# Kernel tuning notes

Hardware: AMD Instinct MI355X
Metric: run time of the kernel (lower is better)

## Reference

```python
import jax, jax.numpy as jnp
import numpy as np
import math

MARGIN = 0.5
SCALE = 64.0
CURVATURE = 1.0
COS_M = math.cos(MARGIN)
SIN_M = math.sin(MARGIN)
TH = math.cos(math.pi - MARGIN)
MM = math.sin(math.pi - MARGIN) * MARGIN

B, D, C = 2048, 512, 16384


def setup_inputs() -> dict:
    key = jax.random.key(0)
    k1, k2, k3 = jax.random.split(key, 3)
    embeddings = jax.random.normal(k1, (B, D), dtype=jnp.float32) * 0.05  # roughly inside the ball
    labels = jax.random.randint(k2, (B,), 0, C)
    # xavier_uniform for [C, D]
    limit = math.sqrt(6.0 / (C + D))
    weight = jax.random.uniform(k3, (C, D), dtype=jnp.float32, minval=-limit, maxval=limit)
    return {"embeddings": embeddings, "labels": labels, "weight": weight}


def _exp_map_zero(v, c):
    sqrt_c = c ** 0.5
    v_norm = jnp.maximum(jnp.linalg.norm(v, axis=-1, keepdims=True), 1e-7)
    return jnp.tanh(sqrt_c * v_norm) * v / (sqrt_c * v_norm)


def reference(embeddings, labels, weight):
    c = CURVATURE
    # class prototypes mapped onto the Poincare ball, clipped to radius 0.95
    proto = _exp_map_zero(weight, c)                                  # [C, D]
    proto_norm = jnp.linalg.norm(proto, axis=-1, keepdims=True)
    proto = jnp.where(proto_norm > 0.95, proto * 0.95 / proto_norm, proto)

    x = embeddings                                                     # [B, D]
    x_sq = jnp.sum(x * x, axis=-1)                                    # [B]
    y_sq = jnp.sum(proto * proto, axis=-1)                            # [C]
    xy = x @ proto.T                                                  # [B, C]
    diff_sq = jnp.maximum(x_sq[:, None] + y_sq[None, :] - 2.0 * xy, 0.0)

    x_sq_c = jnp.minimum(x_sq, 1.0 - 1e-5)
    y_sq_c = jnp.minimum(y_sq, 1.0 - 1e-5)
    denom = (1.0 - c * x_sq_c)[:, None] * (1.0 - c * y_sq_c)[None, :]
    arg = 1.0 + 2.0 * c * diff_sq / jnp.maximum(denom, 1e-7)
    dists = jnp.arccosh(jnp.maximum(arg, 1.0 + 1e-7)) / (c ** 0.5)    # [B, C]

    sims = jnp.exp(-dists)
    cosine = jnp.clip(2.0 * sims - 1.0, -1.0, 1.0)
    sine = jnp.sqrt(jnp.maximum(1.0 - cosine * cosine, 1e-7))
    phi = cosine * COS_M - sine * SIN_M
    phi = jnp.where(cosine > TH, phi, cosine - MM)

    one_hot = jax.nn.one_hot(labels, cosine.shape[1], dtype=cosine.dtype)
    logits = (one_hot * phi + (1.0 - one_hot) * cosine) * SCALE        # [B, C]

    logp = jax.nn.log_softmax(logits, axis=-1)
    loss = -jnp.mean(jnp.take_along_axis(logp, labels[:, None], axis=1))
    return loss
```

## Files before the change

### kernel.cpp

```cpp
#include <hip/hip_runtime.h>
#include <hip/hip_bf16.h>
#include <math.h>

#define Bn 2048
#define Dn 512
#define Cn 16384

typedef __bf16 v8bf __attribute__((ext_vector_type(8)));
typedef float v4f __attribute__((ext_vector_type(4)));

#define WG_BARRIER() asm volatile("s_waitcnt lgkmcnt(0)\n\ts_barrier" ::: "memory")

__global__ __launch_bounds__(256) void prep_kernel(
    const float* __restrict__ w, const float* __restrict__ x,
    __hip_bfloat16* __restrict__ wbf, __hip_bfloat16* __restrict__ xbf,
    float* __restrict__ fscale, float* __restrict__ ysqA, float* __restrict__ yrA,
    float* __restrict__ xsA, float* __restrict__ xrA)
{
  int gw = (blockIdx.x * 256 + threadIdx.x) >> 6;
  int lane = threadIdx.x & 63;
  bool isW = gw < Cn;
  const float* src = isW ? (w + (size_t)gw * Dn) : (x + (size_t)(gw - Cn) * Dn);
  const float4* s4 = (const float4*)src;
  float4 a = s4[lane * 2], b = s4[lane * 2 + 1];
  float ss = a.x * a.x + a.y * a.y + a.z * a.z + a.w * a.w
           + b.x * b.x + b.y * b.y + b.z * b.z + b.w * b.w;
  #pragma unroll
  for (int d = 1; d < 64; d <<= 1) ss += __shfl_xor(ss, d);

  union { __hip_bfloat16 h[8]; int4 i4; } u;
  u.h[0] = __float2bfloat16(a.x); u.h[1] = __float2bfloat16(a.y);
  u.h[2] = __float2bfloat16(a.z); u.h[3] = __float2bfloat16(a.w);
  u.h[4] = __float2bfloat16(b.x); u.h[5] = __float2bfloat16(b.y);
  u.h[6] = __float2bfloat16(b.z); u.h[7] = __float2bfloat16(b.w);
  __hip_bfloat16* dst = isW ? (wbf + (size_t)gw * Dn) : (xbf + (size_t)(gw - Cn) * Dn);
  ((int4*)dst)[lane] = u.i4;

  if (lane == 0) {
    if (isW) {
      float n = fmaxf(sqrtf(ss), 1e-7f);
      float t = tanhf(n);
      float tc = fminf(t, 0.95f);
      fscale[gw] = tc / n;
      float ys = tc * tc;
      ysqA[gw] = ys;
      yrA[gw] = 1.f / (1.f - fminf(ys, 1.f - 1e-5f));
    } else {
      int r = gw - Cn;
      xsA[r] = ss;
      xrA[r] = 1.f / (1.f - fminf(ss, 1.f - 1e-5f));
    }
  }
}

__global__ __launch_bounds__(256) void gemm_kernel(
    const __hip_bfloat16* __restrict__ xbf, const __hip_bfloat16* __restrict__ wbf,
    const float* __restrict__ fscale, const float* __restrict__ ysqA,
    const float* __restrict__ yrA, const float* __restrict__ xsA,
    const float* __restrict__ xrA, float* __restrict__ partials)
{
  __shared__ int4 ldsv[2048];
  char* lds = (char*)ldsv;

  const int bid = blockIdx.x;
  const int xcd = bid & 7;
  const int loc = bid >> 3;
  const int mt  = loc & 15;
  const int nt  = (xcd << 4) | (loc >> 4);
  const int mBase = mt * 128;
  const int nBase = nt * 128;
  const int tid = threadIdx.x;
  const int lane = tid & 63;
  const int wave = tid >> 6;
  const int quad = lane >> 4;
  const int l16 = lane & 15;
  const int waveM = wave >> 1;
  const int waveN = wave & 1;

  v4f acc[4][4];
  #pragma unroll
  for (int i = 0; i < 4; ++i)
    #pragma unroll
    for (int j = 0; j < 4; ++j)
      acc[i][j] = (v4f){0.f, 0.f, 0.f, 0.f};

  const int r0 = tid >> 2,          c0g = tid & 3;
  const int r1 = (tid + 256) >> 2,  c1g = tid & 3;
  const char* gA0 = (const char*)xbf + (size_t)(mBase + r0) * (Dn * 2) + c0g * 16;
  const char* gA1 = (const char*)xbf + (size_t)(mBase + r1) * (Dn * 2) + c1g * 16;
  const char* gW0 = (const char*)wbf + (size_t)(nBase + r0) * (Dn * 2) + c0g * 16;
  const char* gW1 = (const char*)wbf + (size_t)(nBase + r1) * (Dn * 2) + c1g * 16;
  const int lo0 = r0 * 64 + ((c0g ^ (r0 & 3)) * 16);
  const int lo1 = r1 * 64 + ((c1g ^ (r1 & 3)) * 16);

  int aoffs[4], boffs[4];
  #pragma unroll
  for (int i = 0; i < 4; ++i) {
    int ra = waveM * 64 + i * 16 + l16;
    aoffs[i] = ra * 64 + ((quad ^ (ra & 3)) * 16);
    int rb = waveN * 64 + i * 16 + l16;
    boffs[i] = rb * 64 + ((quad ^ (rb & 3)) * 16);
  }

  int4 tA[2][2], tW[2][2];
  tA[0][0] = *(const int4*)gA0;        tA[0][1] = *(const int4*)gA1;
  tW[0][0] = *(const int4*)gW0;        tW[0][1] = *(const int4*)gW1;
  *(int4*)(lds + lo0) = tA[0][0];      *(int4*)(lds + lo1) = tA[0][1];
  *(int4*)(lds + 8192 + lo0) = tW[0][0]; *(int4*)(lds + 8192 + lo1) = tW[0][1];
  tA[1][0] = *(const int4*)(gA0 + 64);  tA[1][1] = *(const int4*)(gA1 + 64);
  tW[1][0] = *(const int4*)(gW0 + 64);  tW[1][1] = *(const int4*)(gW1 + 64);
  tA[0][0] = *(const int4*)(gA0 + 128); tA[0][1] = *(const int4*)(gA1 + 128);
  tW[0][0] = *(const int4*)(gW0 + 128); tW[0][1] = *(const int4*)(gW1 + 128);

  #pragma unroll
  for (int kt = 0; kt < 16; ++kt) {
    const int cur = kt & 1;
    WG_BARRIER();
    const char* Ab = lds + cur * 16384;
    const char* Wb = Ab + 8192;
    v8bf af[4], bfr[4];
    #pragma unroll
    for (int i = 0; i < 4; ++i) af[i] = *(const v8bf*)(Ab + aoffs[i]);
    #pragma unroll
    for (int j = 0; j < 4; ++j) bfr[j] = *(const v8bf*)(Wb + boffs[j]);
    if (kt < 15) {
      const int par = (kt + 1) & 1;
      char* An = lds + (cur ^ 1) * 16384;
      *(int4*)(An + lo0) = tA[par][0];
      *(int4*)(An + lo1) = tA[par][1];
      *(int4*)(An + 8192 + lo0) = tW[par][0];
      *(int4*)(An + 8192 + lo1) = tW[par][1];
      if (kt + 3 < 16) {
        tA[par][0] = *(const int4*)(gA0 + (kt + 3) * 64);
        tA[par][1] = *(const int4*)(gA1 + (kt + 3) * 64);
        tW[par][0] = *(const int4*)(gW0 + (kt + 3) * 64);
        tW[par][1] = *(const int4*)(gW1 + (kt + 3) * 64);
      }
    }
    #pragma unroll
    for (int i = 0; i < 4; ++i)
      #pragma unroll
      for (int j = 0; j < 4; ++j)
        acc[i][j] = __builtin_amdgcn_mfma_f32_16x16x32_bf16(af[i], bfr[j], acc[i][j], 0, 0, 0);
  }

  float ysqj[4], yrj[4], gj[4];
  #pragma unroll
  for (int j = 0; j < 4; ++j) {
    int col = nBase + waveN * 64 + j * 16 + l16;
    gj[j] = -2.f * fscale[col];
    ysqj[j] = ysqA[col];
    yrj[j] = yrA[col];
  }
  #pragma unroll
  for (int i = 0; i < 4; ++i) {
    #pragma unroll
    for (int r = 0; r < 4; ++r) {
      int row = mBase + waveM * 64 + i * 16 + quad * 4 + r;
      float xs = xsA[row];
      float xr2 = 2.f * xrA[row];
      float partial = 0.f;
      if (xs >= 0.99999f) {
        #pragma unroll
        for (int j = 0; j < 4; ++j) {
          float d = fmaxf(fmaf(gj[j], acc[i][j][r], xs + ysqj[j]), 0.f);
          float z = fmaf(d, xr2 * yrj[j], 1.f);
          float u = 64.f * __builtin_amdgcn_rcpf(z);
          partial += fmaf(u, fmaf(0.5f, u, 1.f), 1.f);
        }
      } else {
        #pragma unroll
        for (int j = 0; j < 4; ++j) {
          float d = fmaxf(fmaf(gj[j], acc[i][j][r], xs + ysqj[j]), 0.f);
          float z = fmaf(d, xr2 * yrj[j], 1.f);
          float sq = sqrtf(fmaf(z, z, -1.f));
          float u = 128.f * __builtin_amdgcn_rcpf(z + sq);
          partial += __expf(u);
        }
      }
      partial += __shfl_xor(partial, 1);
      partial += __shfl_xor(partial, 2);
      partial += __shfl_xor(partial, 4);
      partial += __shfl_xor(partial, 8);
      if (l16 == 0) partials[(size_t)row * 256 + nt * 2 + waveN] = partial;
    }
  }
}

__global__ __launch_bounds__(256) void final_kernel(
    const float* __restrict__ x, const float* __restrict__ w,
    const int* __restrict__ labels, const float* __restrict__ fscale,
    const float* __restrict__ ysqA, const float* __restrict__ yrA,
    const float* __restrict__ xsA, const float* __restrict__ xrA,
    const float* __restrict__ partials, float* __restrict__ out)
{
  int row = blockIdx.x * 4 + (threadIdx.x >> 6);
  int lane = threadIdx.x & 63;
  const float* pr = partials + (size_t)row * 256;
  float sum = pr[lane] + pr[lane + 64] + pr[lane + 128] + pr[lane + 192];

  int lab = labels[row];
  const float4* xv = (const float4*)(x + (size_t)row * Dn);
  const float4* wv = (const float4*)(w + (size_t)lab * Dn);
  float4 a0 = xv[lane * 2], a1 = xv[lane * 2 + 1];
  float4 b0 = wv[lane * 2], b1 = wv[lane * 2 + 1];
  float dot = a0.x * b0.x + a0.y * b0.y + a0.z * b0.z + a0.w * b0.w
            + a1.x * b1.x + a1.y * b1.y + a1.z * b1.z + a1.w * b1.w;
  #pragma unroll
  for (int d = 1; d < 64; d <<= 1) {
    sum += __shfl_xor(sum, d);
    dot += __shfl_xor(dot, d);
  }

  __shared__ float red[4];
  if (lane == 0) {
    float xy = fscale[lab] * dot;
    float diff = fmaxf(xsA[row] + ysqA[lab] - 2.f * xy, 0.f);
    float z = fmaf(2.f * diff, xrA[row] * yrA[lab], 1.f);
    float sq = sqrtf(fmaf(z, z, -1.f));
    float sims = 1.f / (z + sq);
    float u_lab = 128.f * sims;
    float cosv = fmaf(2.f, sims, -1.f);
    float sine = sqrtf(fmaxf(fmaf(-cosv, cosv, 1.f), 1e-7f));
    float phi = (cosv > -0.8775825619f)
                    ? (cosv * 0.8775825619f - sine * 0.4794255386f)
                    : (cosv - 0.2397127693f);
    float e_lab = __expf(u_lab);
    float e_phi = __expf(fminf(64.f * phi + 64.f, 80.f));
    red[threadIdx.x >> 6] = logf(sum - e_lab + e_phi) - 64.f * phi - 64.f;
  }
  __syncthreads();
  if (threadIdx.x == 0)
    atomicAdd(out, (red[0] + red[1] + red[2] + red[3]) * (1.f / (float)Bn));
}

extern "C" void kernel_launch(void* const* d_in, const int* in_sizes, int n_in,
                              void* d_out, int out_size, void* d_ws, size_t ws_size,
                              hipStream_t stream) {
  (void)in_sizes; (void)n_in; (void)out_size; (void)ws_size;
  const float* emb = (const float*)d_in[0];
  const int* labels = (const int*)d_in[1];
  const float* weight = (const float*)d_in[2];
  float* out = (float*)d_out;

  char* p = (char*)d_ws;
  __hip_bfloat16* wbf = (__hip_bfloat16*)p; p += (size_t)Cn * Dn * 2;
  __hip_bfloat16* xbf = (__hip_bfloat16*)p; p += (size_t)Bn * Dn * 2;
  float* fscale = (float*)p; p += (size_t)Cn * 4;
  float* ysqA  = (float*)p; p += (size_t)Cn * 4;
  float* yrA   = (float*)p; p += (size_t)Cn * 4;
  float* xsA   = (float*)p; p += (size_t)Bn * 4;
  float* xrA   = (float*)p; p += (size_t)Bn * 4;
  float* partials = (float*)p; p += (size_t)Bn * 256 * 4;

  hipMemsetAsync(out, 0, sizeof(float), stream);
  prep_kernel<<<(Cn + Bn) / 4, 256, 0, stream>>>(weight, emb, wbf, xbf, fscale, ysqA, yrA, xsA, xrA);
  gemm_kernel<<<(Bn / 128) * (Cn / 128), 256, 0, stream>>>(
      xbf, wbf, fscale, ysqA, yrA, xsA, xrA, partials);
  final_kernel<<<Bn / 4, 256, 0, stream>>>(emb, weight, labels, fscale, ysqA, yrA, xsA, xrA, partials, out);
}
```

Baseline: 148.0 us.

## Stream GEMM tiles into LDS with async global_load_lds double buffering

Replaces the register-staged global-to-LDS copy in the fused distance GEMM with direct global_load_lds transfers into a double-buffered LDS ring, prefetching two k-steps ahead. The XOR swizzle moves from the LDS write address to the global read address, and synchronization becomes vmcnt waits plus barriers. This is meant to free registers and VALU/LDS-write instructions and to overlap loads with MFMA. In exchange it adds an extra barrier per k-step, and the fixed vmcnt(4) count ties correctness to the compiler emitting no other vector memory ops in the loop.

Result: faster. 141.6 us (-4.3%).

```diff
diff --git a/kernel.cpp b/kernel.cpp
--- a/kernel.cpp
+++ b/kernel.cpp
@@ -9,7 +9,16 @@
 typedef __bf16 v8bf __attribute__((ext_vector_type(8)));
 typedef float v4f __attribute__((ext_vector_type(4)));
 
-#define WG_BARRIER() asm volatile("s_waitcnt lgkmcnt(0)\n\ts_barrier" ::: "memory")
+#define WAIT_VM4()      asm volatile("s_waitcnt vmcnt(4)" ::: "memory")
+#define WAIT_VM0()      asm volatile("s_waitcnt vmcnt(0)" ::: "memory")
+#define RAW_BAR()       asm volatile("s_barrier" ::: "memory")
+#define LGKM0_BAR()     asm volatile("s_waitcnt lgkmcnt(0)\n\ts_barrier" ::: "memory")
+
+__device__ __forceinline__ void async16(const void* g, void* l) {
+  __builtin_amdgcn_global_load_lds(
+      (const __attribute__((address_space(1))) char*)g,
+      (__attribute__((address_space(3))) char*)l, 16, 0, 0);
+}
 
 __global__ __launch_bounds__(256) void prep_kernel(
     const float* __restrict__ w, const float* __restrict__ x,
@@ -84,14 +93,14 @@
     for (int j = 0; j < 4; ++j)
       acc[i][j] = (v4f){0.f, 0.f, 0.f, 0.f};
 
-  const int r0 = tid >> 2,          c0g = tid & 3;
-  const int r1 = (tid + 256) >> 2,  c1g = tid & 3;
-  const char* gA0 = (const char*)xbf + (size_t)(mBase + r0) * (Dn * 2) + c0g * 16;
-  const char* gA1 = (const char*)xbf + (size_t)(mBase + r1) * (Dn * 2) + c1g * 16;
-  const char* gW0 = (const char*)wbf + (size_t)(nBase + r0) * (Dn * 2) + c0g * 16;
-  const char* gW1 = (const char*)wbf + (size_t)(nBase + r1) * (Dn * 2) + c1g * 16;
-  const int lo0 = r0 * 64 + ((c0g ^ (r0 & 3)) * 16);
-  const int lo1 = r1 * 64 + ((c1g ^ (r1 & 3)) * 16);
+  const int s0 = tid, s1 = tid + 256;
+  const int r0 = s0 >> 2, c0 = (s0 & 3) ^ (r0 & 3);
+  const int r1 = s1 >> 2, c1 = (s1 & 3) ^ (r1 & 3);
+  const char* gA0 = (const char*)xbf + (size_t)(mBase + r0) * (Dn * 2) + c0 * 16;
+  const char* gA1 = (const char*)xbf + (size_t)(mBase + r1) * (Dn * 2) + c1 * 16;
+  const char* gW0 = (const char*)wbf + (size_t)(nBase + r0) * (Dn * 2) + c0 * 16;
+  const char* gW1 = (const char*)wbf + (size_t)(nBase + r1) * (Dn * 2) + c1 * 16;
+  const int lo0 = s0 * 16, lo1 = s1 * 16;
 
   int aoffs[4], boffs[4];
   #pragma unroll
@@ -102,40 +111,33 @@
     boffs[i] = rb * 64 + ((quad ^ (rb & 3)) * 16);
   }
 
-  int4 tA[2][2], tW[2][2];
-  tA[0][0] = *(const int4*)gA0;        tA[0][1] = *(const int4*)gA1;
-  tW[0][0] = *(const int4*)gW0;        tW[0][1] = *(const int4*)gW1;
-  *(int4*)(lds + lo0) = tA[0][0];      *(int4*)(lds + lo1) = tA[0][1];
-  *(int4*)(lds + 8192 + lo0) = tW[0][0]; *(int4*)(lds + 8192 + lo1) = tW[0][1];
-  tA[1][0] = *(const int4*)(gA0 + 64);  tA[1][1] = *(const int4*)(gA1 + 64);
-  tW[1][0] = *(const int4*)(gW0 + 64);  tW[1][1] = *(const int4*)(gW1 + 64);
-  tA[0][0] = *(const int4*)(gA0 + 128); tA[0][1] = *(const int4*)(gA1 + 128);
-  tW[0][0] = *(const int4*)(gW0 + 128); tW[0][1] = *(const int4*)(gW1 + 128);
+  #pragma unroll
+  for (int t = 0; t < 2; ++t) {
+    char* b = lds + t * 16384;
+    async16(gA0 + t * 64, b + lo0);
+    async16(gA1 + t * 64, b + lo1);
+    async16(gW0 + t * 64, b + 8192 + lo0);
+    async16(gW1 + t * 64, b + 8192 + lo1);
+  }
 
   #pragma unroll
   for (int kt = 0; kt < 16; ++kt) {
     const int cur = kt & 1;
-    WG_BARRIER();
-    const char* Ab = lds + cur * 16384;
-    const char* Wb = Ab + 8192;
+    if (kt < 15) { WAIT_VM4(); } else { WAIT_VM0(); }
+    RAW_BAR();
+    char* Ab = lds + cur * 16384;
+    char* Wb = Ab + 8192;
     v8bf af[4], bfr[4];
     #pragma unroll
     for (int i = 0; i < 4; ++i) af[i] = *(const v8bf*)(Ab + aoffs[i]);
     #pragma unroll
     for (int j = 0; j < 4; ++j) bfr[j] = *(const v8bf*)(Wb + boffs[j]);
-    if (kt < 15) {
-      const int par = (kt + 1) & 1;
-      char* An = lds + (cur ^ 1) * 16384;
-      *(int4*)(An + lo0) = tA[par][0];
-      *(int4*)(An + lo1) = tA[par][1];
-      *(int4*)(An + 8192 + lo0) = tW[par][0];
-      *(int4*)(An + 8192 + lo1) = tW[par][1];
-      if (kt + 3 < 16) {
-        tA[par][0] = *(const int4*)(gA0 + (kt + 3) * 64);
-        tA[par][1] = *(const int4*)(gA1 + (kt + 3) * 64);
-        tW[par][0] = *(const int4*)(gW0 + (kt + 3) * 64);
-        tW[par][1] = *(const int4*)(gW1 + (kt + 3) * 64);
-      }
+    LGKM0_BAR();
+    if (kt + 2 < 16) {
+      async16(gA0 + (kt + 2) * 64, Ab + lo0);
+      async16(gA1 + (kt + 2) * 64, Ab + lo1);
+      async16(gW0 + (kt + 2) * 64, Wb + lo0);
+      async16(gW1 + (kt + 2) * 64, Wb + lo1);
     }
     #pragma unroll
     for (int i = 0; i < 4; ++i)
```
